# Optimization experiments

Hardware: AMD Instinct MI355X
Metric: run time of the kernel (lower is better)

Reference implementation:

```python
import jax, jax.numpy as jnp
import numpy as np

CHEB = jnp.array([676.5203681218851, -1259.1392167224028, 771.3234287776531,
                  -176.6150291621406, 12.507343278686905, -0.13857109526572012,
                  9.984369578019572e-06, 1.5056327351493116e-07], dtype=jnp.float32)
TWO_PI = float(np.sqrt(2.0 * np.pi))  # sqrt(2*pi), matches torch two_pi constant


def _gamma(z):
    # Lanczos approximation, 8 Chebyshev terms
    x = jnp.full_like(z, 0.9999999999998099)
    for i in range(8):
        x = x + CHEB[i] / (z + (i + 1.0))
    t = z + 8.0 - 0.5
    y = TWO_PI * t ** (z + 0.5) * jnp.exp(-t) * x
    return y / z


def _lower_incl_gamma(s, x, iters=8):
    it = iters - 2
    gs = _gamma(s)
    L = x ** s * gs * jnp.exp(-x)
    gs = gs * s
    R = jnp.reciprocal(gs) * jnp.ones_like(x)
    X = x
    for k in range(it):
        gs = gs * (s + k + 1)
        R = R + X / gs
        X = X * x
    gs = gs * (s + it + 1)
    R = R + X / gs
    return L * R


def _trigamma(x):
    z = x + 1.0
    zz = z * z
    a = 0.2 - jnp.reciprocal(7.0 * zz)
    b = 1.0 - a / zz
    c = 1.0 + b / (3.0 * z)
    d = 1.0 + c / (2.0 * z)
    return d / z + jnp.reciprocal(x * x)


def _k_update(k, s):
    nm = jnp.log(k) - jax.scipy.special.digamma(k) - s
    dn = jnp.reciprocal(k) - _trigamma(k)
    return k - nm / dn


def _compute_ml_est(x, i=10):
    # x: [B, N]; returns per-image k, th of shape [B]
    x = x + 1e-07
    mean_x = jnp.mean(x, axis=1)
    s = jnp.log(mean_x) - jnp.mean(jnp.log(x), axis=1)
    s3 = s - 3.0
    rt = jnp.sqrt(s3 * s3 + 24.0 * s)
    k = (3.0 - s + rt) / (12.0 * s) + 1e-07
    for _ in range(i):
        k = _k_update(k, s)
    k = jnp.clip(k, 1e-07, 18.0)
    th = jnp.reciprocal(k) * mean_x
    return k, th


def setup_inputs() -> dict:
    key = jax.random.key(0)
    x = jax.random.uniform(key, (256, 224, 224), dtype=jnp.float32)
    return {"x": x}


def reference(x):
    B, H, W = x.shape
    xf = x.reshape(B, H * W)
    xf = xf - jnp.min(xf, axis=1, keepdims=True) + 1e-07
    k, th = _compute_ml_est(xf)            # [B], [B]
    kb = k[:, None]                         # broadcast per-image stats over pixels
    y = jnp.reciprocal(_gamma(kb)) * _lower_incl_gamma(kb, xf / th[:, None])
    y = jnp.where(jnp.isfinite(y), y, jnp.zeros_like(y))
    return y.reshape(B, H, W)
```

## Files before the change

kernel.cpp:

```cpp
#include <hip/hip_runtime.h>
#include <math.h>

#define HW   50176
#define NV4  12544
#define TPB  1024

__device__ __forceinline__ float waveReduceMin(float v) {
#pragma unroll
    for (int o = 32; o > 0; o >>= 1) v = fminf(v, __shfl_down(v, o, 64));
    return v;
}
__device__ __forceinline__ double waveReduceSum(double v) {
#pragma unroll
    for (int o = 32; o > 0; o >>= 1) v += __shfl_down(v, o, 64);
    return v;
}

__device__ __forceinline__ float digamma_f(float x) {
    float r = 0.0f;
    while (x < 6.0f) { r -= 1.0f / x; x += 1.0f; }
    float f = 1.0f / (x * x);
    float ser = f * (1.0f/12.0f - f * (1.0f/120.0f - f * (1.0f/252.0f - f * (1.0f/240.0f - f * (1.0f/132.0f)))));
    return r + logf(x) - 0.5f / x - ser;
}

__device__ __forceinline__ float trigamma_ref(float x) {
    float z = x + 1.0f;
    float zz = z * z;
    float a = 0.2f - 1.0f / (7.0f * zz);
    float b = 1.0f - a / zz;
    float c = 1.0f + b / (3.0f * z);
    float d = 1.0f + c / (2.0f * z);
    return d / z + 1.0f / (x * x);
}

__global__ void __launch_bounds__(TPB)
gamma_norm2d(const float* __restrict__ x, float* __restrict__ out) {
    const int row = blockIdx.x;
    const int tid = threadIdx.x;
    const float4* __restrict__ xr = (const float4*)(x + (size_t)row * HW);
    float4* __restrict__ yr = (float4*)(out + (size_t)row * HW);

    const bool lastValid = (tid < (NV4 - 12 * TPB));

    float4 v[13];
#pragma unroll
    for (int j = 0; j < 12; ++j) v[j] = xr[tid + j * TPB];
    if (lastValid) v[12] = xr[tid + 12 * TPB];
    else           v[12] = make_float4(INFINITY, INFINITY, INFINITY, INFINITY);

    float m = INFINITY;
#pragma unroll
    for (int j = 0; j < 13; ++j)
        m = fminf(m, fminf(fminf(v[j].x, v[j].y), fminf(v[j].z, v[j].w)));
    m = waveReduceMin(m);

    __shared__ float  sminw[16];
    __shared__ double ssum[16], ssuml[16];
    __shared__ float  sparams[3];
    __shared__ float  scoef[8];

    const int wid = tid >> 6, lane = tid & 63;
    if (lane == 0) sminw[wid] = m;
    __syncthreads();
    if (tid == 0) {
        float mm = sminw[0];
        for (int i = 1; i < 16; ++i) mm = fminf(mm, sminw[i]);
        sparams[0] = mm;
    }
    __syncthreads();
    const float rmin = sparams[0];

    double lsum = 0.0, lsl = 0.0;
#pragma unroll
    for (int j = 0; j < 13; ++j) {
        if (j < 12 || lastValid) {
            float e0 = v[j].x, e1 = v[j].y, e2 = v[j].z, e3 = v[j].w;
            float xm0 = (e0 - rmin + 1e-7f) + 1e-7f;
            float xm1 = (e1 - rmin + 1e-7f) + 1e-7f;
            float xm2 = (e2 - rmin + 1e-7f) + 1e-7f;
            float xm3 = (e3 - rmin + 1e-7f) + 1e-7f;
            lsum += ((double)xm0 + (double)xm1) + ((double)xm2 + (double)xm3);
            lsl  += ((double)__logf(xm0) + (double)__logf(xm1))
                  + ((double)__logf(xm2) + (double)__logf(xm3));
        }
    }
    lsum = waveReduceSum(lsum);
    lsl  = waveReduceSum(lsl);
    if (lane == 0) { ssum[wid] = lsum; ssuml[wid] = lsl; }
    __syncthreads();

    if (tid == 0) {
        double ts = 0.0, tl = 0.0;
        for (int i = 0; i < 16; ++i) { ts += ssum[i]; tl += ssuml[i]; }
        const double meand = ts / (double)HW;
        const double mlogd = tl / (double)HW;
        float s = (float)(log(meand) - mlogd);

        float s3 = s - 3.0f;
        float rt = sqrtf(s3 * s3 + 24.0f * s);
        float k  = (3.0f - s + rt) / (12.0f * s) + 1e-7f;
        for (int it = 0; it < 10; ++it) {
            float nm = logf(k) - digamma_f(k) - s;
            float dn = 1.0f / k - trigamma_ref(k);
            k = k - nm / dn;
        }
        if (k < 1e-7f) k = 1e-7f;
        if (k > 18.0f) k = 18.0f;

        const double CH[8] = {676.5203681218851, -1259.1392167224028, 771.3234287776531,
                              -176.6150291621406, 12.507343278686905, -0.13857109526572012,
                              9.984369578019572e-06, 1.5056327351493116e-07};
        double z = (double)k;
        double acc = 0.9999999999998099;
        for (int i = 0; i < 8; ++i) acc += CH[i] / (z + (double)(i + 1));
        double t = z + 7.5;
        double g = 2.5066282746310002 * exp((z + 0.5) * log(t) - t) * acc / z;

        double den = g * z;
        scoef[0] = (float)(1.0 / den);
        for (int j = 1; j < 8; ++j) {
            den *= (z + (double)j);
            scoef[j] = (float)(1.0 / den);
        }
        sparams[1] = k;
        sparams[2] = (float)((double)k / meand);
    }
    __syncthreads();

    const float kk    = sparams[1];
    const float invth = sparams[2];
    const float c0 = scoef[0], c1 = scoef[1], c2 = scoef[2], c3 = scoef[3];
    const float c4 = scoef[4], c5 = scoef[5], c6 = scoef[6], c7 = scoef[7];

#pragma unroll
    for (int j = 0; j < 13; ++j) {
        if (j < 12 || lastValid) {
            float e[4] = {v[j].x, v[j].y, v[j].z, v[j].w};
            float o[4];
#pragma unroll
            for (int q = 0; q < 4; ++q) {
                float xf = e[q] - rmin + 1e-7f;
                float xq = xf * invth;
                float p = fmaf(c7, xq, c6);
                p = fmaf(p, xq, c5);
                p = fmaf(p, xq, c4);
                p = fmaf(p, xq, c3);
                p = fmaf(p, xq, c2);
                p = fmaf(p, xq, c1);
                p = fmaf(p, xq, c0);
                float tt = __expf(fmaf(kk, __logf(xq), -xq));
                float y = tt * p;
                o[q] = isfinite(y) ? y : 0.0f;
            }
            yr[tid + j * TPB] = make_float4(o[0], o[1], o[2], o[3]);
        }
    }
}

extern "C" void kernel_launch(void* const* d_in, const int* in_sizes, int n_in,
                              void* d_out, int out_size, void* d_ws, size_t ws_size,
                              hipStream_t stream) {
    const float* x = (const float*)d_in[0];
    float* out = (float*)d_out;
    const int rows = in_sizes[0] / HW;
    gamma_norm2d<<<dim3(rows), dim3(TPB), 0, stream>>>(x, out);
}
```

Baseline: 113.6 us.

## Split fused per-row kernel into five chunked kernels via workspace

```diff
diff --git a/kernel.cpp b/kernel.cpp
--- a/kernel.cpp
+++ b/kernel.cpp
@@ -1,16 +1,23 @@
 #include <hip/hip_runtime.h>
 #include <math.h>
 
-#define HW   50176
-#define NV4  12544
-#define TPB  1024
+#define HW       50176
+#define NV4      12544
+#define CHUNKS   7
+#define CV4      1792
+#define TPB      256
+
+#define WS_SUM(ws)    ((double*)((char*)(ws)))
+#define WS_SUML(ws)   ((double*)((char*)(ws) + 14336))
+#define WS_MIN(ws)    ((float*)((char*)(ws) + 28672))
+#define WS_PAR(ws)    ((float*)((char*)(ws) + 35840))
 
 __device__ __forceinline__ float waveReduceMin(float v) {
 #pragma unroll
     for (int o = 32; o > 0; o >>= 1) v = fminf(v, __shfl_down(v, o, 64));
     return v;
 }
-__device__ __forceinline__ double waveReduceSum(double v) {
+__device__ __forceinline__ double waveReduceSumD(double v) {
 #pragma unroll
     for (int o = 32; o > 0; o >>= 1) v += __shfl_down(v, o, 64);
     return v;
@@ -35,126 +42,166 @@
 }
 
 __global__ void __launch_bounds__(TPB)
-gamma_norm2d(const float* __restrict__ x, float* __restrict__ out) {
-    const int row = blockIdx.x;
-    const int tid = threadIdx.x;
-    const float4* __restrict__ xr = (const float4*)(x + (size_t)row * HW);
-    float4* __restrict__ yr = (float4*)(out + (size_t)row * HW);
-
-    const bool lastValid = (tid < (NV4 - 12 * TPB));
-
-    float4 v[13];
-#pragma unroll
-    for (int j = 0; j < 12; ++j) v[j] = xr[tid + j * TPB];
-    if (lastValid) v[12] = xr[tid + 12 * TPB];
-    else           v[12] = make_float4(INFINITY, INFINITY, INFINITY, INFINITY);
-
-    float m = INFINITY;
-#pragma unroll
-    for (int j = 0; j < 13; ++j)
-        m = fminf(m, fminf(fminf(v[j].x, v[j].y), fminf(v[j].z, v[j].w)));
-    m = waveReduceMin(m);
-
-    __shared__ float  sminw[16];
-    __shared__ double ssum[16], ssuml[16];
-    __shared__ float  sparams[3];
-    __shared__ float  scoef[8];
-
+k1_stats(const float* __restrict__ x, void* __restrict__ ws) {
+    const int bid  = blockIdx.x;
+    const int row  = bid / CHUNKS;
+    const int chnk = bid - row * CHUNKS;
+    const int tid  = threadIdx.x;
+    const float4* __restrict__ xr =
+        (const float4*)(x) + (size_t)row * NV4 + (size_t)chnk * CV4;
+
+    float pmin = INFINITY;
+    float psum = 0.0f;
+    float psl  = 0.0f;
+#pragma unroll
+    for (int j = 0; j < 7; ++j) {
+        float4 v = xr[j * TPB + tid];
+        pmin = fminf(pmin, fminf(fminf(v.x, v.y), fminf(v.z, v.w)));
+        psum += (v.x + v.y) + (v.z + v.w);
+        (void)psl;
+    }
+    pmin = waveReduceMin(pmin);
+    double dsum = waveReduceSumD((double)psum);
+
+    __shared__ float  smin[4];
+    __shared__ double ssum[4];
     const int wid = tid >> 6, lane = tid & 63;
-    if (lane == 0) sminw[wid] = m;
+    if (lane == 0) { smin[wid] = pmin; ssum[wid] = dsum; }
     __syncthreads();
     if (tid == 0) {
-        float mm = sminw[0];
-        for (int i = 1; i < 16; ++i) mm = fminf(mm, sminw[i]);
-        sparams[0] = mm;
-    }
+        float mm = fminf(fminf(smin[0], smin[1]), fminf(smin[2], smin[3]));
+        double ss = (ssum[0] + ssum[1]) + (ssum[2] + ssum[3]);
+        WS_MIN(ws)[bid] = mm;
+        WS_SUM(ws)[bid] = ss;
+    }
+}
+
+__global__ void __launch_bounds__(64)
+k1b_min(void* __restrict__ ws) {
+    const int row = blockIdx.x * 64 + threadIdx.x;
+    if (row >= 256) return;
+    const float* mins = WS_MIN(ws);
+    float mm = INFINITY;
+#pragma unroll
+    for (int i = 0; i < CHUNKS; ++i) mm = fminf(mm, mins[row * CHUNKS + i]);
+    WS_PAR(ws)[row * 12 + 0] = mm;
+}
+
+__global__ void __launch_bounds__(TPB)
+k1c_sumlog(const float* __restrict__ x, void* __restrict__ ws) {
+    const int bid  = blockIdx.x;
+    const int row  = bid / CHUNKS;
+    const int chnk = bid - row * CHUNKS;
+    const int tid  = threadIdx.x;
+    const float rmin = WS_PAR(ws)[row * 12 + 0];
+    const float4* __restrict__ xr =
+        (const float4*)(x) + (size_t)row * NV4 + (size_t)chnk * CV4;
+
+    float psl = 0.0f;
+#pragma unroll
+    for (int j = 0; j < 7; ++j) {
+        float4 v = xr[j * TPB + tid];
+        float a0 = (v.x - rmin + 1e-7f) + 1e-7f;
+        float a1 = (v.y - rmin + 1e-7f) + 1e-7f;
+        float a2 = (v.z - rmin + 1e-7f) + 1e-7f;
+        float a3 = (v.w - rmin + 1e-7f) + 1e-7f;
+        psl += (__logf(a0) + __logf(a1)) + (__logf(a2) + __logf(a3));
+    }
+    double dsl = waveReduceSumD((double)psl);
+    __shared__ double ssl[4];
+    const int wid = tid >> 6, lane = tid & 63;
+    if (lane == 0) ssl[wid] = dsl;
     __syncthreads();
-    const float rmin = sparams[0];
-
-    double lsum = 0.0, lsl = 0.0;
-#pragma unroll
-    for (int j = 0; j < 13; ++j) {
-        if (j < 12 || lastValid) {
-            float e0 = v[j].x, e1 = v[j].y, e2 = v[j].z, e3 = v[j].w;
-            float xm0 = (e0 - rmin + 1e-7f) + 1e-7f;
-            float xm1 = (e1 - rmin + 1e-7f) + 1e-7f;
-            float xm2 = (e2 - rmin + 1e-7f) + 1e-7f;
-            float xm3 = (e3 - rmin + 1e-7f) + 1e-7f;
-            lsum += ((double)xm0 + (double)xm1) + ((double)xm2 + (double)xm3);
-            lsl  += ((double)__logf(xm0) + (double)__logf(xm1))
-                  + ((double)__logf(xm2) + (double)__logf(xm3));
+    if (tid == 0)
+        WS_SUML(ws)[bid] = (ssl[0] + ssl[1]) + (ssl[2] + ssl[3]);
+}
+
+__global__ void __launch_bounds__(64)
+k2_solve(void* __restrict__ ws) {
+    const int row = blockIdx.x * 64 + threadIdx.x;
+    if (row >= 256) return;
+    float* par = WS_PAR(ws) + row * 12;
+    const float rmin = par[0];
+
+    double ts = 0.0, tl = 0.0;
+#pragma unroll
+    for (int i = 0; i < CHUNKS; ++i) {
+        ts += WS_SUM(ws)[row * CHUNKS + i];
+        tl += WS_SUML(ws)[row * CHUNKS + i];
+    }
+    ts = ts - (double)HW * ((double)rmin - 2e-7);
+    const double meand = ts / (double)HW;
+    const double mlogd = tl / (double)HW;
+    float s = (float)(log(meand) - mlogd);
+
+    float s3 = s - 3.0f;
+    float rt = sqrtf(s3 * s3 + 24.0f * s);
+    float k  = (3.0f - s + rt) / (12.0f * s) + 1e-7f;
+    for (int it = 0; it < 10; ++it) {
+        float nm = logf(k) - digamma_f(k) - s;
+        float dn = 1.0f / k - trigamma_ref(k);
+        k = k - nm / dn;
+    }
+    if (k < 1e-7f) k = 1e-7f;
+    if (k > 18.0f) k = 18.0f;
+
+    const double CH[8] = {676.5203681218851, -1259.1392167224028, 771.3234287776531,
+                          -176.6150291621406, 12.507343278686905, -0.13857109526572012,
+                          9.984369578019572e-06, 1.5056327351493116e-07};
+    double z = (double)k;
+    double acc = 0.9999999999998099;
+#pragma unroll
+    for (int i = 0; i < 8; ++i) acc += CH[i] / (z + (double)(i + 1));
+    double t = z + 7.5;
+    double g = 2.5066282746310002 * exp((z + 0.5) * log(t) - t) * acc / z;
+
+    double den = g * z;
+    par[1] = k;
+    par[2] = (float)((double)k / meand);
+    par[3] = (float)(1.0 / den);
+#pragma unroll
+    for (int j = 1; j < 8; ++j) {
+        den *= (z + (double)j);
+        par[3 + j] = (float)(1.0 / den);
+    }
+}
+
+__global__ void __launch_bounds__(TPB)
+k3_apply(const float* __restrict__ x, float* __restrict__ out,
+         const void* __restrict__ ws) {
+    const int bid  = blockIdx.x;
+    const int row  = bid / CHUNKS;
+    const int chnk = bid - row * CHUNKS;
+    const int tid  = threadIdx.x;
+    const float* par = WS_PAR((void*)ws) + row * 12;
+    const float rmin = par[0], kk = par[1], invth = par[2];
+    const float c0 = par[3], c1 = par[4], c2 = par[5], c3 = par[6];
+    const float c4 = par[7], c5 = par[8], c6 = par[9], c7 = par[10];
+
+    const size_t base = (size_t)row * NV4 + (size_t)chnk * CV4;
+    const float4* __restrict__ xr = (const float4*)(x) + base;
+    float4* __restrict__ yr = (float4*)(out) + base;
+
+#pragma unroll
+    for (int j = 0; j < 7; ++j) {
+        float4 v = xr[j * TPB + tid];
+        float e[4] = {v.x, v.y, v.z, v.w};
+        float o[4];
+#pragma unroll
+        for (int q = 0; q < 4; ++q) {
+            float xq = (e[q] - rmin + 1e-7f) * invth;
+            float p = fmaf(c7, xq, c6);
+            p = fmaf(p, xq, c5);
+            p = fmaf(p, xq, c4);
+            p = fmaf(p, xq, c3);
+            p = fmaf(p, xq, c2);
+            p = fmaf(p, xq, c1);
+            p = fmaf(p, xq, c0);
+            float tt = __expf(fmaf(kk, __logf(xq), -xq));
+            float y = tt * p;
+            o[q] = isfinite(y) ? y : 0.0f;
         }
-    }
-    lsum = waveReduceSum(lsum);
-    lsl  = waveReduceSum(lsl);
-    if (lane == 0) { ssum[wid] = lsum; ssuml[wid] = lsl; }
-    __syncthreads();
-
-    if (tid == 0) {
-        double ts = 0.0, tl = 0.0;
-        for (int i = 0; i < 16; ++i) { ts += ssum[i]; tl += ssuml[i]; }
-        const double meand = ts / (double)HW;
-        const double mlogd = tl / (double)HW;
-        float s = (float)(log(meand) - mlogd);
-
-        float s3 = s - 3.0f;
-        float rt = sqrtf(s3 * s3 + 24.0f * s);
-        float k  = (3.0f - s + rt) / (12.0f * s) + 1e-7f;
-        for (int it = 0; it < 10; ++it) {
-            float nm = logf(k) - digamma_f(k) - s;
-            float dn = 1.0f / k - trigamma_ref(k);
-            k = k - nm / dn;
-        }
-        if (k < 1e-7f) k = 1e-7f;
-        if (k > 18.0f) k = 18.0f;
-
-        const double CH[8] = {676.5203681218851, -1259.1392167224028, 771.3234287776531,
-                              -176.6150291621406, 12.507343278686905, -0.13857109526572012,
-                              9.984369578019572e-06, 1.5056327351493116e-07};
-        double z = (double)k;
-        double acc = 0.9999999999998099;
-        for (int i = 0; i < 8; ++i) acc += CH[i] / (z + (double)(i + 1));
-        double t = z + 7.5;
-        double g = 2.5066282746310002 * exp((z + 0.5) * log(t) - t) * acc / z;
-
-        double den = g * z;
-        scoef[0] = (float)(1.0 / den);
-        for (int j = 1; j < 8; ++j) {
-            den *= (z + (double)j);
-            scoef[j] = (float)(1.0 / den);
-        }
-        sparams[1] = k;
-        sparams[2] = (float)((double)k / meand);
-    }
-    __syncthreads();
-
-    const float kk    = sparams[1];
-    const float invth = sparams[2];
-    const float c0 = scoef[0], c1 = scoef[1], c2 = scoef[2], c3 = scoef[3];
-    const float c4 = scoef[4], c5 = scoef[5], c6 = scoef[6], c7 = scoef[7];
-
-#pragma unroll
-    for (int j = 0; j < 13; ++j) {
-        if (j < 12 || lastValid) {
-            float e[4] = {v[j].x, v[j].y, v[j].z, v[j].w};
-            float o[4];
-#pragma unroll
-            for (int q = 0; q < 4; ++q) {
-                float xf = e[q] - rmin + 1e-7f;
-                float xq = xf * invth;
-                float p = fmaf(c7, xq, c6);
-                p = fmaf(p, xq, c5);
-                p = fmaf(p, xq, c4);
-                p = fmaf(p, xq, c3);
-                p = fmaf(p, xq, c2);
-                p = fmaf(p, xq, c1);
-                p = fmaf(p, xq, c0);
-                float tt = __expf(fmaf(kk, __logf(xq), -xq));
-                float y = tt * p;
-                o[q] = isfinite(y) ? y : 0.0f;
-            }
-            yr[tid + j * TPB] = make_float4(o[0], o[1], o[2], o[3]);
-        }
+        yr[j * TPB + tid] = make_float4(o[0], o[1], o[2], o[3]);
     }
 }
 
@@ -164,5 +211,11 @@
     const float* x = (const float*)d_in[0];
     float* out = (float*)d_out;
     const int rows = in_sizes[0] / HW;
-    gamma_norm2d<<<dim3(rows), dim3(TPB), 0, stream>>>(x, out);
-}
+    const int nchunk = rows * CHUNKS;
+
+    k1_stats  <<<dim3(nchunk), dim3(TPB), 0, stream>>>(x, d_ws);
+    k1b_min   <<<dim3((rows + 63) / 64), dim3(64), 0, stream>>>(d_ws);
+    k1c_sumlog<<<dim3(nchunk), dim3(TPB), 0, stream>>>(x, d_ws);
+    k2_solve  <<<dim3((rows + 63) / 64), dim3(64), 0, stream>>>(d_ws);
+    k3_apply  <<<dim3(nchunk), dim3(TPB), 0, stream>>>(x, out, d_ws);
+}
```

New measurement: 124.9 us. 10.0% more time.

## Split each row across four blocks with cooperative grid sync reductions

Applied to the files above, without the earlier changes.

```diff
diff --git a/kernel.cpp b/kernel.cpp
--- a/kernel.cpp
+++ b/kernel.cpp
@@ -1,16 +1,29 @@
 #include <hip/hip_runtime.h>
+#include <hip/hip_cooperative_groups.h>
 #include <math.h>
 
-#define HW   50176
-#define NV4  12544
-#define TPB  1024
-
-__device__ __forceinline__ float waveReduceMin(float v) {
+namespace cg = cooperative_groups;
+
+#define HW    50176
+#define NV4   12544
+#define ROWS  256
+#define CPR   4
+#define CV4   3136
+#define TPB   256
+#define NBLK  (ROWS * CPR)
+
+typedef float floatx4 __attribute__((ext_vector_type(4)));
+
+#define WS_MIN(ws)  ((float*)(ws))
+#define WS_SUM(ws)  ((double*)((char*)(ws) + 4096))
+#define WS_SL(ws)   ((double*)((char*)(ws) + 12288))
+
+__device__ __forceinline__ float waveMin(float v) {
 #pragma unroll
     for (int o = 32; o > 0; o >>= 1) v = fminf(v, __shfl_down(v, o, 64));
     return v;
 }
-__device__ __forceinline__ double waveReduceSum(double v) {
+__device__ __forceinline__ double waveSumD(double v) {
 #pragma unroll
     for (int o = 32; o > 0; o >>= 1) v += __shfl_down(v, o, 64);
     return v;
@@ -23,10 +36,8 @@
     float ser = f * (1.0f/12.0f - f * (1.0f/120.0f - f * (1.0f/252.0f - f * (1.0f/240.0f - f * (1.0f/132.0f)))));
     return r + logf(x) - 0.5f / x - ser;
 }
-
 __device__ __forceinline__ float trigamma_ref(float x) {
-    float z = x + 1.0f;
-    float zz = z * z;
+    float z = x + 1.0f, zz = z * z;
     float a = 0.2f - 1.0f / (7.0f * zz);
     float b = 1.0f - a / zz;
     float c = 1.0f + b / (3.0f * z);
@@ -34,126 +45,231 @@
     return d / z + 1.0f / (x * x);
 }
 
-__global__ void __launch_bounds__(TPB)
-gamma_norm2d(const float* __restrict__ x, float* __restrict__ out) {
-    const int row = blockIdx.x;
-    const int tid = threadIdx.x;
-    const float4* __restrict__ xr = (const float4*)(x + (size_t)row * HW);
-    float4* __restrict__ yr = (float4*)(out + (size_t)row * HW);
-
-    const bool lastValid = (tid < (NV4 - 12 * TPB));
+__device__ __forceinline__ void solve_params(double ts, double tl, float rmin, float* par) {
+    ts -= (double)HW * ((double)rmin - 2e-7);
+    const double meand = ts / (double)HW;
+    float s = (float)(log(meand) - tl / (double)HW);
+
+    float s3 = s - 3.0f;
+    float rt = sqrtf(s3 * s3 + 24.0f * s);
+    float k  = (3.0f - s + rt) / (12.0f * s) + 1e-7f;
+    for (int it = 0; it < 10; ++it) {
+        float nm = logf(k) - digamma_f(k) - s;
+        float dn = 1.0f / k - trigamma_ref(k);
+        k = k - nm / dn;
+    }
+    if (k < 1e-7f) k = 1e-7f;
+    if (k > 18.0f) k = 18.0f;
+
+    const double CH[8] = {676.5203681218851, -1259.1392167224028, 771.3234287776531,
+                          -176.6150291621406, 12.507343278686905, -0.13857109526572012,
+                          9.984369578019572e-06, 1.5056327351493116e-07};
+    double z = (double)k;
+    double acc = 0.9999999999998099;
+#pragma unroll
+    for (int i = 0; i < 8; ++i) acc += CH[i] / (z + (double)(i + 1));
+    double t = z + 7.5;
+    double g = 2.5066282746310002 * exp((z + 0.5) * log(t) - t) * acc / z;
+
+    par[0] = k;
+    par[1] = (float)((double)k / meand);
+    double den = g * z;
+    par[2] = (float)(1.0 / den);
+#pragma unroll
+    for (int j = 1; j < 8; ++j) {
+        den *= (z + (double)j);
+        par[2 + j] = (float)(1.0 / den);
+    }
+}
+
+__device__ __forceinline__ float apply_one(float e, float rmin, float invth,
+                                           float kk, const float* c) {
+    float xq = (e - rmin + 1e-7f) * invth;
+    float p = fmaf(c[7], xq, c[6]);
+    p = fmaf(p, xq, c[5]);
+    p = fmaf(p, xq, c[4]);
+    p = fmaf(p, xq, c[3]);
+    p = fmaf(p, xq, c[2]);
+    p = fmaf(p, xq, c[1]);
+    p = fmaf(p, xq, c[0]);
+    float y = __expf(fmaf(kk, __logf(xq), -xq)) * p;
+    return isfinite(y) ? y : 0.0f;
+}
+
+__global__ void __launch_bounds__(TPB, 4)
+gamma_coop(const float* __restrict__ x, float* __restrict__ out, void* __restrict__ ws) {
+    cg::grid_group grid = cg::this_grid();
+    const int bid  = blockIdx.x;
+    const int row  = bid >> 2;
+    const int chnk = bid & 3;
+    const int tid  = threadIdx.x;
+    const int wid  = tid >> 6, lane = tid & 63;
+    const bool extra = (tid < (CV4 - 12 * TPB));
+
+    const size_t base = (size_t)row * NV4 + (size_t)chnk * CV4;
+    const float4* __restrict__ xr = (const float4*)x + base;
 
     float4 v[13];
 #pragma unroll
-    for (int j = 0; j < 12; ++j) v[j] = xr[tid + j * TPB];
-    if (lastValid) v[12] = xr[tid + 12 * TPB];
-    else           v[12] = make_float4(INFINITY, INFINITY, INFINITY, INFINITY);
-
-    float m = INFINITY;
-#pragma unroll
-    for (int j = 0; j < 13; ++j)
-        m = fminf(m, fminf(fminf(v[j].x, v[j].y), fminf(v[j].z, v[j].w)));
-    m = waveReduceMin(m);
-
-    __shared__ float  sminw[16];
-    __shared__ double ssum[16], ssuml[16];
-    __shared__ float  sparams[3];
-    __shared__ float  scoef[8];
-
+    for (int j = 0; j < 12; ++j) v[j] = xr[j * TPB + tid];
+    v[12] = extra ? xr[12 * TPB + tid]
+                  : make_float4(INFINITY, INFINITY, INFINITY, INFINITY);
+
+    float pmin = INFINITY, psum = 0.0f;
+#pragma unroll
+    for (int j = 0; j < 13; ++j) {
+        pmin = fminf(pmin, fminf(fminf(v[j].x, v[j].y), fminf(v[j].z, v[j].w)));
+        if (j < 12 || extra) psum += (v[j].x + v[j].y) + (v[j].z + v[j].w);
+    }
+    pmin = waveMin(pmin);
+    double dsum = waveSumD((double)psum);
+
+    __shared__ float  smin[4];
+    __shared__ double sacc[4];
+    __shared__ float  spar[10];
+    if (lane == 0) { smin[wid] = pmin; sacc[wid] = dsum; }
+    __syncthreads();
+    if (tid == 0) {
+        WS_MIN(ws)[bid] = fminf(fminf(smin[0], smin[1]), fminf(smin[2], smin[3]));
+        WS_SUM(ws)[bid] = (sacc[0] + sacc[1]) + (sacc[2] + sacc[3]);
+    }
+    grid.sync();
+
+    const float* wm = WS_MIN(ws) + (row << 2);
+    const float rmin = fminf(fminf(wm[0], wm[1]), fminf(wm[2], wm[3]));
+
+    float psl = 0.0f;
+#pragma unroll
+    for (int j = 0; j < 13; ++j) {
+        if (j < 12 || extra) {
+            psl += (__logf(v[j].x - rmin + 1e-7f + 1e-7f) + __logf(v[j].y - rmin + 1e-7f + 1e-7f))
+                 + (__logf(v[j].z - rmin + 1e-7f + 1e-7f) + __logf(v[j].w - rmin + 1e-7f + 1e-7f));
+        }
+    }
+    double dsl = waveSumD((double)psl);
+    if (lane == 0) sacc[wid] = dsl;
+    __syncthreads();
+    if (tid == 0)
+        WS_SL(ws)[bid] = (sacc[0] + sacc[1]) + (sacc[2] + sacc[3]);
+    grid.sync();
+
+    if (tid == 0) {
+        const double* su = WS_SUM(ws) + (row << 2);
+        const double* sl = WS_SL(ws)  + (row << 2);
+        double ts = (su[0] + su[1]) + (su[2] + su[3]);
+        double tl = (sl[0] + sl[1]) + (sl[2] + sl[3]);
+        solve_params(ts, tl, rmin, spar);
+    }
+    __syncthreads();
+    const float kk = spar[0], invth = spar[1];
+    float c[8];
+#pragma unroll
+    for (int i = 0; i < 8; ++i) c[i] = spar[2 + i];
+
+    floatx4* __restrict__ yr = (floatx4*)out + base;
+#pragma unroll
+    for (int j = 0; j < 13; ++j) {
+        if (j < 12 || extra) {
+            floatx4 o;
+            o.x = apply_one(v[j].x, rmin, invth, kk, c);
+            o.y = apply_one(v[j].y, rmin, invth, kk, c);
+            o.z = apply_one(v[j].z, rmin, invth, kk, c);
+            o.w = apply_one(v[j].w, rmin, invth, kk, c);
+            __builtin_nontemporal_store(o, yr + j * TPB + tid);
+        }
+    }
+}
+
+__global__ void __launch_bounds__(TPB, 4)
+k_phaseA(const float* __restrict__ x, void* __restrict__ ws) {
+    const int bid = blockIdx.x, tid = threadIdx.x;
+    const int row = bid >> 2, chnk = bid & 3;
     const int wid = tid >> 6, lane = tid & 63;
-    if (lane == 0) sminw[wid] = m;
-    __syncthreads();
-    if (tid == 0) {
-        float mm = sminw[0];
-        for (int i = 1; i < 16; ++i) mm = fminf(mm, sminw[i]);
-        sparams[0] = mm;
-    }
-    __syncthreads();
-    const float rmin = sparams[0];
-
-    double lsum = 0.0, lsl = 0.0;
-#pragma unroll
-    for (int j = 0; j < 13; ++j) {
-        if (j < 12 || lastValid) {
-            float e0 = v[j].x, e1 = v[j].y, e2 = v[j].z, e3 = v[j].w;
-            float xm0 = (e0 - rmin + 1e-7f) + 1e-7f;
-            float xm1 = (e1 - rmin + 1e-7f) + 1e-7f;
-            float xm2 = (e2 - rmin + 1e-7f) + 1e-7f;
-            float xm3 = (e3 - rmin + 1e-7f) + 1e-7f;
-            lsum += ((double)xm0 + (double)xm1) + ((double)xm2 + (double)xm3);
-            lsl  += ((double)__logf(xm0) + (double)__logf(xm1))
-                  + ((double)__logf(xm2) + (double)__logf(xm3));
-        }
-    }
-    lsum = waveReduceSum(lsum);
-    lsl  = waveReduceSum(lsl);
-    if (lane == 0) { ssum[wid] = lsum; ssuml[wid] = lsl; }
-    __syncthreads();
-
-    if (tid == 0) {
-        double ts = 0.0, tl = 0.0;
-        for (int i = 0; i < 16; ++i) { ts += ssum[i]; tl += ssuml[i]; }
-        const double meand = ts / (double)HW;
-        const double mlogd = tl / (double)HW;
-        float s = (float)(log(meand) - mlogd);
-
-        float s3 = s - 3.0f;
-        float rt = sqrtf(s3 * s3 + 24.0f * s);
-        float k  = (3.0f - s + rt) / (12.0f * s) + 1e-7f;
-        for (int it = 0; it < 10; ++it) {
-            float nm = logf(k) - digamma_f(k) - s;
-            float dn = 1.0f / k - trigamma_ref(k);
-            k = k - nm / dn;
-        }
-        if (k < 1e-7f) k = 1e-7f;
-        if (k > 18.0f) k = 18.0f;
-
-        const double CH[8] = {676.5203681218851, -1259.1392167224028, 771.3234287776531,
-                              -176.6150291621406, 12.507343278686905, -0.13857109526572012,
-                              9.984369578019572e-06, 1.5056327351493116e-07};
-        double z = (double)k;
-        double acc = 0.9999999999998099;
-        for (int i = 0; i < 8; ++i) acc += CH[i] / (z + (double)(i + 1));
-        double t = z + 7.5;
-        double g = 2.5066282746310002 * exp((z + 0.5) * log(t) - t) * acc / z;
-
-        double den = g * z;
-        scoef[0] = (float)(1.0 / den);
-        for (int j = 1; j < 8; ++j) {
-            den *= (z + (double)j);
-            scoef[j] = (float)(1.0 / den);
-        }
-        sparams[1] = k;
-        sparams[2] = (float)((double)k / meand);
-    }
-    __syncthreads();
-
-    const float kk    = sparams[1];
-    const float invth = sparams[2];
-    const float c0 = scoef[0], c1 = scoef[1], c2 = scoef[2], c3 = scoef[3];
-    const float c4 = scoef[4], c5 = scoef[5], c6 = scoef[6], c7 = scoef[7];
-
-#pragma unroll
-    for (int j = 0; j < 13; ++j) {
-        if (j < 12 || lastValid) {
-            float e[4] = {v[j].x, v[j].y, v[j].z, v[j].w};
-            float o[4];
-#pragma unroll
-            for (int q = 0; q < 4; ++q) {
-                float xf = e[q] - rmin + 1e-7f;
-                float xq = xf * invth;
-                float p = fmaf(c7, xq, c6);
-                p = fmaf(p, xq, c5);
-                p = fmaf(p, xq, c4);
-                p = fmaf(p, xq, c3);
-                p = fmaf(p, xq, c2);
-                p = fmaf(p, xq, c1);
-                p = fmaf(p, xq, c0);
-                float tt = __expf(fmaf(kk, __logf(xq), -xq));
-                float y = tt * p;
-                o[q] = isfinite(y) ? y : 0.0f;
-            }
-            yr[tid + j * TPB] = make_float4(o[0], o[1], o[2], o[3]);
+    const bool extra = (tid < (CV4 - 12 * TPB));
+    const float4* __restrict__ xr = (const float4*)x + (size_t)row * NV4 + (size_t)chnk * CV4;
+
+    float pmin = INFINITY, psum = 0.0f;
+#pragma unroll
+    for (int j = 0; j < 13; ++j) {
+        if (j < 12 || extra) {
+            float4 v = xr[j * TPB + tid];
+            pmin = fminf(pmin, fminf(fminf(v.x, v.y), fminf(v.z, v.w)));
+            psum += (v.x + v.y) + (v.z + v.w);
+        }
+    }
+    pmin = waveMin(pmin);
+    double dsum = waveSumD((double)psum);
+    __shared__ float  smin[4];
+    __shared__ double sacc[4];
+    if (lane == 0) { smin[wid] = pmin; sacc[wid] = dsum; }
+    __syncthreads();
+    if (tid == 0) {
+        WS_MIN(ws)[bid] = fminf(fminf(smin[0], smin[1]), fminf(smin[2], smin[3]));
+        WS_SUM(ws)[bid] = (sacc[0] + sacc[1]) + (sacc[2] + sacc[3]);
+    }
+}
+
+__global__ void __launch_bounds__(TPB, 4)
+k_phaseB(const float* __restrict__ x, void* __restrict__ ws) {
+    const int bid = blockIdx.x, tid = threadIdx.x;
+    const int row = bid >> 2, chnk = bid & 3;
+    const int wid = tid >> 6, lane = tid & 63;
+    const bool extra = (tid < (CV4 - 12 * TPB));
+    const float* wm = WS_MIN(ws) + (row << 2);
+    const float rmin = fminf(fminf(wm[0], wm[1]), fminf(wm[2], wm[3]));
+    const float4* __restrict__ xr = (const float4*)x + (size_t)row * NV4 + (size_t)chnk * CV4;
+
+    float psl = 0.0f;
+#pragma unroll
+    for (int j = 0; j < 13; ++j) {
+        if (j < 12 || extra) {
+            float4 v = xr[j * TPB + tid];
+            psl += (__logf(v.x - rmin + 1e-7f + 1e-7f) + __logf(v.y - rmin + 1e-7f + 1e-7f))
+                 + (__logf(v.z - rmin + 1e-7f + 1e-7f) + __logf(v.w - rmin + 1e-7f + 1e-7f));
+        }
+    }
+    double dsl = waveSumD((double)psl);
+    __shared__ double sacc[4];
+    if (lane == 0) sacc[wid] = dsl;
+    __syncthreads();
+    if (tid == 0) WS_SL(ws)[bid] = (sacc[0] + sacc[1]) + (sacc[2] + sacc[3]);
+}
+
+__global__ void __launch_bounds__(TPB, 4)
+k_phaseC(const float* __restrict__ x, float* __restrict__ out, void* __restrict__ ws) {
+    const int bid = blockIdx.x, tid = threadIdx.x;
+    const int row = bid >> 2, chnk = bid & 3;
+    const bool extra = (tid < (CV4 - 12 * TPB));
+    const float* wm = WS_MIN(ws) + (row << 2);
+    const float rmin = fminf(fminf(wm[0], wm[1]), fminf(wm[2], wm[3]));
+
+    __shared__ float spar[10];
+    if (tid == 0) {
+        const double* su = WS_SUM(ws) + (row << 2);
+        const double* sl = WS_SL(ws)  + (row << 2);
+        double ts = (su[0] + su[1]) + (su[2] + su[3]);
+        double tl = (sl[0] + sl[1]) + (sl[2] + sl[3]);
+        solve_params(ts, tl, rmin, spar);
+    }
+    __syncthreads();
+    const float kk = spar[0], invth = spar[1];
+    float c[8];
+#pragma unroll
+    for (int i = 0; i < 8; ++i) c[i] = spar[2 + i];
+
+    const size_t base = (size_t)row * NV4 + (size_t)chnk * CV4;
+    const float4* __restrict__ xr = (const float4*)x + base;
+    floatx4* __restrict__ yr = (floatx4*)out + base;
+#pragma unroll
+    for (int j = 0; j < 13; ++j) {
+        if (j < 12 || extra) {
+            float4 v = xr[j * TPB + tid];
+            floatx4 o;
+            o.x = apply_one(v.x, rmin, invth, kk, c);
+            o.y = apply_one(v.y, rmin, invth, kk, c);
+            o.z = apply_one(v.z, rmin, invth, kk, c);
+            o.w = apply_one(v.w, rmin, invth, kk, c);
+            __builtin_nontemporal_store(o, yr + j * TPB + tid);
         }
     }
 }
@@ -163,6 +279,15 @@
                               hipStream_t stream) {
     const float* x = (const float*)d_in[0];
     float* out = (float*)d_out;
-    const int rows = in_sizes[0] / HW;
-    gamma_norm2d<<<dim3(rows), dim3(TPB), 0, stream>>>(x, out);
-}
+    void* ws = d_ws;
+
+    void* args[] = {(void*)&x, (void*)&out, (void*)&ws};
+    hipError_t err = hipLaunchCooperativeKernel((const void*)gamma_coop,
+                                                dim3(NBLK), dim3(TPB), args, 0, stream);
+    if (err != hipSuccess) {
+        (void)hipGetLastError();
+        k_phaseA<<<dim3(NBLK), dim3(TPB), 0, stream>>>(x, ws);
+        k_phaseB<<<dim3(NBLK), dim3(TPB), 0, stream>>>(x, ws);
+        k_phaseC<<<dim3(NBLK), dim3(TPB), 0, stream>>>(x, out, ws);
+    }
+}
```

After: 321.0 us. +182.5%, slower.
